# Performance work log

Hardware: AMD Instinct MI355X
Metric: run time of the kernel (lower is better)

## Reference

```python
import jax, jax.numpy as jnp
import numpy as np

B, S_ENC, T_DEC, I, H = 1024, 49, 25, 76, 2048  # S_ENC = source_seq_len - 1


def setup_inputs() -> dict:
    key = jax.random.key(0)
    ks = jax.random.split(key, 6)
    sc = 0.02
    return {
        "encoder_inputs": jax.random.normal(ks[0], (B, S_ENC, I), jnp.float32),
        "decoder_inputs": jax.random.normal(ks[1], (B, T_DEC, I), jnp.float32),
        "W_ih": jax.random.normal(ks[2], (3 * H, I), jnp.float32) * sc,
        "W_hh": jax.random.normal(ks[3], (3 * H, H), jnp.float32) * sc,
        "b_ih": jnp.zeros((3 * H,), jnp.float32),
        "b_hh": jnp.zeros((3 * H,), jnp.float32),
        "fc_w": jax.random.normal(ks[4], (I, H), jnp.float32) * sc,
        "fc_b": jnp.zeros((I,), jnp.float32),
    }


def gru_cell(x, h, W_ih, W_hh, b_ih, b_hh):
    # PyTorch GRUCell: gates stacked [r; z; n] along first axis of weights.
    gi = x @ W_ih.T + b_ih  # [B, 3H]
    gh = h @ W_hh.T + b_hh  # [B, 3H]
    i_r, i_z, i_n = jnp.split(gi, 3, axis=-1)
    h_r, h_z, h_n = jnp.split(gh, 3, axis=-1)
    r = jax.nn.sigmoid(i_r + h_r)
    z = jax.nn.sigmoid(i_z + h_z)
    n = jnp.tanh(i_n + r * h_n)
    return (1.0 - z) * n + z * h


def reference(encoder_inputs, decoder_inputs, W_ih, W_hh, b_ih, b_hh, fc_w, fc_b):
    # Dropout p=0.0 (and eval mode) -> identity; omitted.
    h0 = jnp.zeros((encoder_inputs.shape[0], H), encoder_inputs.dtype)
    enc = jnp.swapaxes(encoder_inputs, 0, 1)  # [S_ENC, B, I]

    def enc_step(h, x):
        return gru_cell(x, h, W_ih, W_hh, b_ih, b_hh), None

    h, _ = jax.lax.scan(enc_step, h0, enc)

    # Sampling-based decoding: only decoder_inputs[:, 0] is consumed; every
    # later step feeds back the previous output. Each step's input is detached.
    prev0 = decoder_inputs[:, 0, :]

    def dec_step(carry, _):
        h, prev = carry
        inp = jax.lax.stop_gradient(prev)  # inp.detach() in the torch code
        h_new = gru_cell(inp, h, W_ih, W_hh, b_ih, b_hh)
        out = inp + h_new @ fc_w.T + fc_b  # residual over fc1 projection
        return (h_new, out), out

    _, outs = jax.lax.scan(dec_step, (h, prev0), None, length=T_DEC)
    return jnp.swapaxes(outs, 0, 1)  # [B, T_DEC, I]
```

## Files before the change

kernel.cpp:

```cpp
#include <hip/hip_runtime.h>
#include <cstdint>
#include <cstddef>

#define DI __device__ __forceinline__

typedef __bf16 bf16x8 __attribute__((ext_vector_type(8)));
typedef float  f32x4  __attribute__((ext_vector_type(4)));
typedef unsigned short ushort_t;

constexpr int BATCH = 1024;
constexpr int HID   = 2048;
constexpr int IN    = 76;
constexpr int SENC  = 49;
constexpr int TDEC  = 25;
constexpr int KX    = 128;
constexpr int KP    = KX + HID;
constexpr int BK    = 64;
constexpr int KTT   = KP / BK;
constexpr int OSTR  = TDEC * IN;

DI unsigned short f2bf(float f) {
  union { float f; unsigned u; } v; v.f = f;
  unsigned u = v.u;
  return (unsigned short)((u + 0x7fffu + ((u >> 16) & 1u)) >> 16);
}

DI float bf2f(unsigned short h) {
  union { unsigned u; float f; } v; v.u = ((unsigned)h) << 16;
  return v.f;
}

DI f32x4 mfma16(bf16x8 a, bf16x8 b, f32x4 c) {
  return __builtin_amdgcn_mfma_f32_16x16x32_bf16(a, b, c, 0, 0, 0);
}

DI void gload_lds16(const void* g, void* l) {
  __builtin_amdgcn_global_load_lds((const __attribute__((address_space(1))) void*)g,
                                   (__attribute__((address_space(3))) void*)l,
                                   16, 0, 0);
}

DI float sigmoidf_(float x) { return 1.0f / (1.0f + __expf(-x)); }
DI float tanhf_(float x)    { return 1.0f - 2.0f / (1.0f + __expf(2.0f * x)); }


__global__ void pack_W(const float* __restrict__ Wih, const float* __restrict__ Whh,
                       ushort_t* __restrict__ Wp) {
  int idx = blockIdx.x * 256 + threadIdx.x;
  if (idx >= 6144 * KP) return;
  int n = idx / KP;
  int k = idx - n * KP;
  float v = 0.f;
  if (k < IN)        v = Wih[(size_t)n * IN + k];
  else if (k >= KX)  v = Whh[(size_t)n * HID + (k - KX)];
  Wp[idx] = f2bf(v);
}

__global__ void pack_xe(const float* __restrict__ enc, ushort_t* __restrict__ xe) {
  int idx = blockIdx.x * 256 + threadIdx.x;
  if (idx >= SENC * BATCH * KX) return;
  int t = idx >> 17;
  int rem = idx & 131071;
  int b = rem >> 7, k = rem & 127;
  float v = (k < IN) ? enc[(size_t)b * (SENC * IN) + t * IN + k] : 0.f;
  xe[idx] = f2bf(v);
}

__global__ void pack_xd0(const float* __restrict__ dec, ushort_t* __restrict__ xd) {
  int idx = blockIdx.x * 256 + threadIdx.x;
  if (idx >= BATCH * KX) return;
  int b = idx >> 7, k = idx & 127;
  float v = (k < IN) ? dec[(size_t)b * OSTR + k] : 0.f;
  xd[idx] = f2bf(v);
}

__global__ void pack_fc(const float* __restrict__ fcw, ushort_t* __restrict__ Wfc) {
  int idx = blockIdx.x * 256 + threadIdx.x;
  if (idx >= 80 * HID) return;
  int n = idx >> 11, k = idx & 2047;
  float v = (n < IN) ? fcw[(size_t)n * HID + k] : 0.f;
  Wfc[idx] = f2bf(v);
}

__global__ __launch_bounds__(128, 2) void gru_step_kernel(
    const ushort_t* __restrict__ x,
    const ushort_t* __restrict__ hbp,
    const ushort_t* __restrict__ Wp,
    const float*    __restrict__ b_ih,
    const float*    __restrict__ b_hh,
    ushort_t*       __restrict__ hbn)
{
  __shared__ ushort_t lds[2][(64 + 96) * BK];

  const int tid  = threadIdx.x;
  const int lane = tid & 63;
  const int wid  = tid >> 6;
  const int bid  = blockIdx.x;
  const int xcd   = bid & 7;
  const int idx   = bid >> 3;
  const int m_grp = idx & 15;
  const int n_grp = xcd + 8 * (idx >> 4);
  const int row0  = m_grp * 64;
  const int col0  = n_grp * 32;
  const int wn = wid;

  const f32x4 Z4 = {0.f, 0.f, 0.f, 0.f};
  f32x4 accr[4], accz[4], accN[4], accin[4];
  #pragma unroll
  for (int a = 0; a < 4; ++a) { accr[a] = Z4; accz[a] = Z4; accN[a] = Z4; accin[a] = Z4; }

  const int srow  = lane >> 3;
  const int swcol = (((lane & 7) ^ (srow & 7)) << 3);

  const int lr  = lane & 15;
  const int lhi = lane >> 4;
  const int bc  = lhi * 16;
  const int ksw0 = ((bc)      ^ ((lane & 7) << 4)) >> 1;
  const int ksw1 = ((64 + bc) ^ ((lane & 7) << 4)) >> 1;

  auto stage = [&](int buf, int kt) {
    const ushort_t* asrc; int astr, ak0;
    if (kt < 2) { asrc = x;   astr = KX;  ak0 = kt * BK; }
    else        { asrc = hbp; astr = HID; ak0 = (kt - 2) * BK; }
    ushort_t* Lb = &lds[buf][0];
    #pragma unroll
    for (int c = 0; c < 4; ++c) {
      const int chunk = wid * 4 + c;
      const ushort_t* g = asrc + (size_t)(row0 + chunk * 8 + srow) * astr + ak0 + swcol;
      gload_lds16(g, Lb + chunk * 512);
    }
    const int wk0 = kt * BK;
    #pragma unroll
    for (int c = 0; c < 6; ++c) {
      const int chunk = wid * 6 + c;
      const int brow = chunk * 8 + srow;
      const int gg = brow >> 5, wi = brow & 31;
      const ushort_t* g = Wp + (size_t)(gg * HID + col0 + wi) * KP + wk0 + swcol;
      gload_lds16(g, Lb + 64 * BK + chunk * 512);
    }
  };

  auto readFrags = [&](const ushort_t* base, int ko, bf16x8 af[4], bf16x8 bg[3]) {
    #pragma unroll
    for (int fm = 0; fm < 4; ++fm)
      af[fm] = *reinterpret_cast<const bf16x8*>(&base[(fm * 16 + lr) * BK + ko]);
    #pragma unroll
    for (int g = 0; g < 3; ++g)
      bg[g] = *reinterpret_cast<const bf16x8*>(
          &base[64 * BK + (g * 32 + wn * 16 + lr) * BK + ko]);
  };

  auto burst = [&](bf16x8 af[4], bf16x8 bg[3]) {
    __builtin_amdgcn_s_setprio(1);
    #pragma unroll
    for (int fm = 0; fm < 4; ++fm) {
      accr[fm] = mfma16(af[fm], bg[0], accr[fm]);
      accz[fm] = mfma16(af[fm], bg[1], accz[fm]);
      accN[fm] = mfma16(af[fm], bg[2], accN[fm]);
    }
    __builtin_amdgcn_s_setprio(0);
  };

  bf16x8 afA[4], bgA[3];
  bf16x8 afB[4], bgB[3];

  stage(0, 0);
  asm volatile("s_waitcnt vmcnt(0)" ::: "memory");
  __builtin_amdgcn_s_barrier();

  for (int kt = 0; kt < KTT; ++kt) {
    const ushort_t* base = &lds[kt & 1][0];
    if (kt + 1 < KTT) stage((kt + 1) & 1, kt + 1);
    readFrags(base, ksw0, afA, bgA);
    readFrags(base, ksw1, afB, bgB);
    burst(afA, bgA);
    burst(afB, bgB);

    if (kt == 1) {
      #pragma unroll
      for (int a = 0; a < 4; ++a) { accin[a] = accN[a]; accN[a] = Z4; }
    }

    if (kt + 1 < KTT) {
      asm volatile("s_waitcnt vmcnt(0)" ::: "memory");
      __builtin_amdgcn_s_barrier();
    }
  }

  const int lqb = lhi * 4;
  const int j = col0 + wn * 16 + lr;
  const float br  = b_ih[j] + b_hh[j];
  const float bz  = b_ih[HID + j] + b_hh[HID + j];
  const float bin = b_ih[2 * HID + j];
  const float bhn = b_hh[2 * HID + j];
  #pragma unroll
  for (int fm = 0; fm < 4; ++fm) {
    #pragma unroll
    for (int q = 0; q < 4; ++q) {
      const int row = row0 + fm * 16 + lqb + q;
      const size_t off = (size_t)row * HID + j;
      const float hp = bf2f(hbp[off]);
      const float rr = sigmoidf_(accr[fm][q] + br);
      const float zz = sigmoidf_(accz[fm][q] + bz);
      const float nn = tanhf_(accin[fm][q] + bin + rr * (accN[fm][q] + bhn));
      const float hv = (1.0f - zz) * nn + zz * hp;
      hbn[off] = f2bf(hv);
    }
  }
}

__global__ __launch_bounds__(512) void fc_kernel(
    const ushort_t* __restrict__ hb,
    const ushort_t* __restrict__ Wfc,
    const float*    __restrict__ fc_b,
    const float*    __restrict__ prev,
    float*          __restrict__ outp,
    ushort_t*       __restrict__ xd)
{
  __shared__ float red[8][16][80];
  const int tid = threadIdx.x, lane = tid & 63, wid = tid >> 6;
  const int r0 = blockIdx.x * 16;
  const int lr = lane & 15, lk = (lane >> 4) * 8;
  const f32x4 Z4 = {0.f, 0.f, 0.f, 0.f};
  f32x4 acc[5];
  #pragma unroll
  for (int f = 0; f < 5; ++f) acc[f] = Z4;
  const int kbase = wid * 256;
  #pragma unroll
  for (int ks = 0; ks < 8; ++ks) {
    const int k = kbase + ks * 32 + lk;
    bf16x8 a = *reinterpret_cast<const bf16x8*>(&hb[(size_t)(r0 + lr) * HID + k]);
    #pragma unroll
    for (int f = 0; f < 5; ++f) {
      bf16x8 b = *reinterpret_cast<const bf16x8*>(&Wfc[(size_t)(f * 16 + lr) * HID + k]);
      acc[f] = mfma16(a, b, acc[f]);
    }
  }
  #pragma unroll
  for (int f = 0; f < 5; ++f)
    #pragma unroll
    for (int q = 0; q < 4; ++q)
      red[wid][(lane >> 4) * 4 + q][f * 16 + lr] = acc[f][q];
  __syncthreads();

  if (tid < 256) {
    const int rowi = tid >> 4;
    const int j0   = (tid & 15) * 8;
    const int b_   = r0 + rowi;
    #pragma unroll
    for (int jj = 0; jj < 8; ++jj) {
      const int j = j0 + jj;
      float ov = 0.f;
      if (j < IN) {
        float s = 0.f;
        #pragma unroll
        for (int w = 0; w < 8; ++w) s += red[w][rowi][j];
        ov = prev[(size_t)b_ * OSTR + j] + fc_b[j] + s;
        outp[(size_t)b_ * OSTR + j] = ov;
      }
      xd[b_ * KX + j] = f2bf(j < IN ? ov : 0.f);
    }
  }
}

extern "C" void kernel_launch(void* const* d_in, const int* in_sizes, int n_in,
                              void* d_out, int out_size, void* d_ws, size_t ws_size,
                              hipStream_t stream) {
  const float* enc = (const float*)d_in[0];
  const float* dec = (const float*)d_in[1];
  const float* Wih = (const float*)d_in[2];
  const float* Whh = (const float*)d_in[3];
  const float* bih = (const float*)d_in[4];
  const float* bhh = (const float*)d_in[5];
  const float* fcw = (const float*)d_in[6];
  const float* fcb = (const float*)d_in[7];
  float* out = (float*)d_out;

  char* ws = (char*)d_ws;
  ushort_t* Wp  = (ushort_t*)ws;  ws += (size_t)6144 * KP * 2;
  ushort_t* xe  = (ushort_t*)ws;  ws += (size_t)SENC * BATCH * KX * 2;
  ushort_t* xd  = (ushort_t*)ws;  ws += (size_t)BATCH * KX * 2;
  ushort_t* Wfc = (ushort_t*)ws;  ws += (size_t)80 * HID * 2;
  ushort_t* hb0 = (ushort_t*)ws;  ws += (size_t)BATCH * HID * 2;
  ushort_t* hb1 = (ushort_t*)ws;  ws += (size_t)BATCH * HID * 2;
  ushort_t* hbp[2] = {hb0, hb1};

  pack_W  <<<(6144 * KP + 255) / 256, 256, 0, stream>>>(Wih, Whh, Wp);
  pack_xe <<<(SENC * BATCH * KX + 255) / 256, 256, 0, stream>>>(enc, xe);
  pack_xd0<<<(BATCH * KX + 255) / 256, 256, 0, stream>>>(dec, xd);
  pack_fc <<<(80 * HID + 255) / 256, 256, 0, stream>>>(fcw, Wfc);
  hipMemsetAsync(hb0, 0, (size_t)BATCH * HID * 2, stream);

  for (int s = 0; s < SENC + TDEC; ++s) {
    const ushort_t* xsrc = (s < SENC) ? (xe + (size_t)s * BATCH * KX) : xd;
    gru_step_kernel<<<1024, 128, 0, stream>>>(xsrc, hbp[s & 1], Wp, bih, bhh,
                                              hbp[(s + 1) & 1]);
    if (s >= SENC) {
      const int t = s - SENC;
      const float* prev = (t == 0) ? dec : (out + (size_t)(t - 1) * IN);
      fc_kernel<<<64, 512, 0, stream>>>(hbp[(s + 1) & 1], Wfc, fcb, prev,
                                        out + (size_t)t * IN, xd);
    }
  }
}
```

Before: 3.003 ms.

## Load GRU weight fragments directly to registers from prepacked MFMA layout

Weights are repacked into an MFMA-fragment-ordered layout so each lane loads its B fragment with one contiguous 16-byte global load into registers, double-buffered across k-steps, instead of staging through LDS. The block tile grows to 128 rows with four waves sharing the weight columns, halving the grid. This removes LDS traffic and bank pressure for weights but puts global-load latency directly on the register pipeline and raises register use.

Result: faster. 2.857 ms (-4.9%).

```diff
diff --git a/kernel.cpp b/kernel.cpp
--- a/kernel.cpp
+++ b/kernel.cpp
@@ -17,6 +17,7 @@
 constexpr int KP    = KX + HID;
 constexpr int BK    = 64;
 constexpr int KTT   = KP / BK;
+constexpr int NKT32 = KP / 32;
 constexpr int OSTR  = TDEC * IN;
 
 DI unsigned short f2bf(float f) {
@@ -44,16 +45,22 @@
 DI float tanhf_(float x)    { return 1.0f - 2.0f / (1.0f + __expf(2.0f * x)); }
 
 
-__global__ void pack_W(const float* __restrict__ Wih, const float* __restrict__ Whh,
-                       ushort_t* __restrict__ Wp) {
+__global__ void pack_Wf(const float* __restrict__ Wih, const float* __restrict__ Whh,
+                        ushort_t* __restrict__ Wf) {
   int idx = blockIdx.x * 256 + threadIdx.x;
   if (idx >= 6144 * KP) return;
-  int n = idx / KP;
-  int k = idx - n * KP;
+  int fid  = idx >> 9;
+  int el   = idx & 511;
+  int lane = el >> 3;
+  int e    = el & 7;
+  int nt   = fid / NKT32;
+  int ktl  = fid - nt * NKT32;
+  int n    = nt * 16 + (lane & 15);
+  int k    = ktl * 32 + (lane >> 4) * 8 + e;
   float v = 0.f;
   if (k < IN)        v = Wih[(size_t)n * IN + k];
   else if (k >= KX)  v = Whh[(size_t)n * HID + (k - KX)];
-  Wp[idx] = f2bf(v);
+  Wf[idx] = f2bf(v);
 }
 
 __global__ void pack_xe(const float* __restrict__ enc, ushort_t* __restrict__ xe) {
@@ -82,15 +89,15 @@
   Wfc[idx] = f2bf(v);
 }
 
-__global__ __launch_bounds__(128, 2) void gru_step_kernel(
+__global__ __launch_bounds__(256, 2) void gru_step_kernel(
     const ushort_t* __restrict__ x,
     const ushort_t* __restrict__ hbp,
-    const ushort_t* __restrict__ Wp,
+    const ushort_t* __restrict__ Wf,
     const float*    __restrict__ b_ih,
     const float*    __restrict__ b_hh,
     ushort_t*       __restrict__ hbn)
 {
-  __shared__ ushort_t lds[2][(64 + 96) * BK];
+  __shared__ ushort_t lds[2][128 * BK];
 
   const int tid  = threadIdx.x;
   const int lane = tid & 63;
@@ -98,11 +105,13 @@
   const int bid  = blockIdx.x;
   const int xcd   = bid & 7;
   const int idx   = bid >> 3;
-  const int m_grp = idx & 15;
-  const int n_grp = xcd + 8 * (idx >> 4);
-  const int row0  = m_grp * 64;
+  const int m_grp = idx & 7;
+  const int n_grp = xcd + 8 * (idx >> 3);
+  const int row0  = m_grp * 128;
   const int col0  = n_grp * 32;
-  const int wn = wid;
+  const int wm = wid >> 1;
+  const int wn = wid & 1;
+  const int NTb = n_grp * 2 + wn;
 
   const f32x4 Z4 = {0.f, 0.f, 0.f, 0.f};
   f32x4 accr[4], accz[4], accN[4], accin[4];
@@ -118,7 +127,7 @@
   const int ksw0 = ((bc)      ^ ((lane & 7) << 4)) >> 1;
   const int ksw1 = ((64 + bc) ^ ((lane & 7) << 4)) >> 1;
 
-  auto stage = [&](int buf, int kt) {
+  auto stageA = [&](int buf, int kt) {
     const ushort_t* asrc; int astr, ak0;
     if (kt < 2) { asrc = x;   astr = KX;  ak0 = kt * BK; }
     else        { asrc = hbp; astr = HID; ak0 = (kt - 2) * BK; }
@@ -129,62 +138,66 @@
       const ushort_t* g = asrc + (size_t)(row0 + chunk * 8 + srow) * astr + ak0 + swcol;
       gload_lds16(g, Lb + chunk * 512);
     }
-    const int wk0 = kt * BK;
-    #pragma unroll
-    for (int c = 0; c < 6; ++c) {
-      const int chunk = wid * 6 + c;
-      const int brow = chunk * 8 + srow;
-      const int gg = brow >> 5, wi = brow & 31;
-      const ushort_t* g = Wp + (size_t)(gg * HID + col0 + wi) * KP + wk0 + swcol;
-      gload_lds16(g, Lb + 64 * BK + chunk * 512);
-    }
-  };
-
-  auto readFrags = [&](const ushort_t* base, int ko, bf16x8 af[4], bf16x8 bg[3]) {
+  };
+
+  auto loadB = [&](int kt, bf16x8 (&bg)[6]) {
+    #pragma unroll
+    for (int g = 0; g < 3; ++g)
+      #pragma unroll
+      for (int ks = 0; ks < 2; ++ks) {
+        const size_t fo = ((size_t)((g * 128 + NTb) * NKT32 + (kt * 2 + ks))) << 9;
+        bg[g * 2 + ks] = *reinterpret_cast<const bf16x8*>(Wf + fo + lane * 8);
+      }
+  };
+
+  auto readA = [&](const ushort_t* base, int ko, bf16x8 af[4]) {
     #pragma unroll
     for (int fm = 0; fm < 4; ++fm)
-      af[fm] = *reinterpret_cast<const bf16x8*>(&base[(fm * 16 + lr) * BK + ko]);
-    #pragma unroll
-    for (int g = 0; g < 3; ++g)
-      bg[g] = *reinterpret_cast<const bf16x8*>(
-          &base[64 * BK + (g * 32 + wn * 16 + lr) * BK + ko]);
-  };
-
-  auto burst = [&](bf16x8 af[4], bf16x8 bg[3]) {
+      af[fm] = *reinterpret_cast<const bf16x8*>(&base[(wm * 64 + fm * 16 + lr) * BK + ko]);
+  };
+
+  auto burst = [&](bf16x8 af[4], bf16x8 br, bf16x8 bz, bf16x8 bn) {
     __builtin_amdgcn_s_setprio(1);
     #pragma unroll
     for (int fm = 0; fm < 4; ++fm) {
-      accr[fm] = mfma16(af[fm], bg[0], accr[fm]);
-      accz[fm] = mfma16(af[fm], bg[1], accz[fm]);
-      accN[fm] = mfma16(af[fm], bg[2], accN[fm]);
+      accr[fm] = mfma16(af[fm], br, accr[fm]);
+      accz[fm] = mfma16(af[fm], bz, accz[fm]);
+      accN[fm] = mfma16(af[fm], bn, accN[fm]);
     }
     __builtin_amdgcn_s_setprio(0);
   };
 
-  bf16x8 afA[4], bgA[3];
-  bf16x8 afB[4], bgB[3];
-
-  stage(0, 0);
+  bf16x8 B0[6], B1[6];
+  bf16x8 afA[4], afB[4];
+
+  loadB(0, B0);
+  stageA(0, 0);
   asm volatile("s_waitcnt vmcnt(0)" ::: "memory");
   __builtin_amdgcn_s_barrier();
 
-  for (int kt = 0; kt < KTT; ++kt) {
+  auto body = [&](int kt, bf16x8 (&Bc)[6], bf16x8 (&Bn)[6]) {
+    if (kt + 1 < KTT) {
+      loadB(kt + 1, Bn);
+      stageA((kt + 1) & 1, kt + 1);
+    }
     const ushort_t* base = &lds[kt & 1][0];
-    if (kt + 1 < KTT) stage((kt + 1) & 1, kt + 1);
-    readFrags(base, ksw0, afA, bgA);
-    readFrags(base, ksw1, afB, bgB);
-    burst(afA, bgA);
-    burst(afB, bgB);
-
+    readA(base, ksw0, afA);
+    readA(base, ksw1, afB);
+    burst(afA, Bc[0], Bc[2], Bc[4]);
+    burst(afB, Bc[1], Bc[3], Bc[5]);
     if (kt == 1) {
       #pragma unroll
       for (int a = 0; a < 4; ++a) { accin[a] = accN[a]; accN[a] = Z4; }
     }
-
     if (kt + 1 < KTT) {
       asm volatile("s_waitcnt vmcnt(0)" ::: "memory");
       __builtin_amdgcn_s_barrier();
     }
+  };
+
+  for (int kt = 0; kt < KTT; kt += 2) {
+    body(kt,     B0, B1);
+    body(kt + 1, B1, B0);
   }
 
   const int lqb = lhi * 4;
@@ -197,7 +210,7 @@
   for (int fm = 0; fm < 4; ++fm) {
     #pragma unroll
     for (int q = 0; q < 4; ++q) {
-      const int row = row0 + fm * 16 + lqb + q;
+      const int row = row0 + wm * 64 + fm * 16 + lqb + q;
       const size_t off = (size_t)row * HID + j;
       const float hp = bf2f(hbp[off]);
       const float rr = sigmoidf_(accr[fm][q] + br);
@@ -277,7 +290,7 @@
   float* out = (float*)d_out;
 
   char* ws = (char*)d_ws;
-  ushort_t* Wp  = (ushort_t*)ws;  ws += (size_t)6144 * KP * 2;
+  ushort_t* Wf  = (ushort_t*)ws;  ws += (size_t)6144 * KP * 2;
   ushort_t* xe  = (ushort_t*)ws;  ws += (size_t)SENC * BATCH * KX * 2;
   ushort_t* xd  = (ushort_t*)ws;  ws += (size_t)BATCH * KX * 2;
   ushort_t* Wfc = (ushort_t*)ws;  ws += (size_t)80 * HID * 2;
@@ -285,7 +298,7 @@
   ushort_t* hb1 = (ushort_t*)ws;  ws += (size_t)BATCH * HID * 2;
   ushort_t* hbp[2] = {hb0, hb1};
 
-  pack_W  <<<(6144 * KP + 255) / 256, 256, 0, stream>>>(Wih, Whh, Wp);
+  pack_Wf <<<(6144 * KP + 255) / 256, 256, 0, stream>>>(Wih, Whh, Wf);
   pack_xe <<<(SENC * BATCH * KX + 255) / 256, 256, 0, stream>>>(enc, xe);
   pack_xd0<<<(BATCH * KX + 255) / 256, 256, 0, stream>>>(dec, xd);
   pack_fc <<<(80 * HID + 255) / 256, 256, 0, stream>>>(fcw, Wfc);
@@ -293,8 +306,8 @@
 
   for (int s = 0; s < SENC + TDEC; ++s) {
     const ushort_t* xsrc = (s < SENC) ? (xe + (size_t)s * BATCH * KX) : xd;
-    gru_step_kernel<<<1024, 128, 0, stream>>>(xsrc, hbp[s & 1], Wp, bih, bhh,
-                                              hbp[(s + 1) & 1]);
+    gru_step_kernel<<<512, 256, 0, stream>>>(xsrc, hbp[s & 1], Wf, bih, bhh,
+                                             hbp[(s + 1) & 1]);
     if (s >= SENC) {
       const int t = s - SENC;
       const float* prev = (t == 0) ? dec : (out + (size_t)(t - 1) * IN);
```
